# Kernel optimization log

Hardware: AMD Instinct MI355X
Metric: run time of the kernel (lower is better)

## Reference

```python
import jax, jax.numpy as jnp
import numpy as np

N_RAYS = 32768
HID = 64
MARCH_ITERS = 64
EPS = 1e-4
NEAR = 0.0
FAR = 1.0
T_FAR = 1.0
TPUT_B = 64
JITTER = 1.0 / TPUT_B  # fixed stand-in for random.random() * (2 / batch_size)


def _init_linear(key, fan_in, fan_out):
    kw, kb = jax.random.split(key)
    lim = 1.0 / np.sqrt(fan_in)
    W = jax.random.uniform(kw, (fan_in, fan_out), jnp.float32, -lim, lim)
    b = jax.random.uniform(kb, (fan_out,), jnp.float32, -lim, lim)
    return W, b


def setup_inputs() -> dict:
    key = jax.random.key(0)
    ks = jax.random.split(key, 6)
    rays = jax.random.normal(ks[0], (N_RAYS, 6), jnp.float32)
    W0, b0 = _init_linear(ks[1], 3, HID)
    W1, b1 = _init_linear(ks[2], HID, HID)
    W2, b2 = _init_linear(ks[3], HID, 1)
    Wr0, br0 = _init_linear(ks[4], 6, HID)
    Wr1, br1 = _init_linear(ks[5], HID, 3)
    return dict(rays=rays, W0=W0, b0=b0, W1=W1, b1=b1, W2=W2, b2=b2,
                Wr0=Wr0, br0=br0, Wr1=Wr1, br1=br1)


def _sdf(p, W0, b0, W1, b1, W2, b2):
    # p: [N, 3] -> signed distance [N, 1]
    h = jax.nn.relu(p @ W0 + b0)
    h = jax.nn.relu(h @ W1 + b1)
    return h @ W2 + b2


def _refl(p, d, Wr0, br0, Wr1, br1):
    # p, d: [N, 3] -> RGB [N, 3]
    h = jax.nn.relu(jnp.concatenate([p, d], axis=-1) @ Wr0 + br0)
    return jax.nn.sigmoid(h @ Wr1 + br1)


def reference(rays, W0, b0, W1, b1, W2, b2, Wr0, br0, Wr1, br1):
    r_o, r_d = rays[..., :3], rays[..., 3:]
    sdf = lambda p: _sdf(p, W0, b0, W1, b1, W2, b2)

    # --- sphere march (64 fixed iterations; early-exit break is a no-op
    # once all rays hit, since hit rays stop updating) ---
    hits0 = jnp.zeros(r_o.shape[:-1] + (1,), jnp.bool_)
    dist0 = jnp.full(r_o.shape[:-1] + (1,), NEAR, jnp.float32)

    def march(carry, _):
        hits, cd = carry
        d = sdf(r_o + r_d * cd)  # [N, 1]
        hits = hits | ((d < EPS) & (cd >= NEAR) & (cd <= FAR))
        cd = jnp.where(~hits, cd + d, cd)
        return (hits, cd), None

    (hit, t), _ = jax.lax.scan(march, (hits0, dist0), None, length=MARCH_ITERS)
    pts = r_o + r_d * t

    rgb = _refl(pts, r_d, Wr0, br0, Wr1, br1)
    rgb = jnp.where(hit, rgb, 0.0)  # out[~hit] = 0

    # --- throughput (index search under no_grad in the original) ---
    max_t = T_FAR + JITTER
    step = max_t / TPUT_B
    sg = jax.lax.stop_gradient
    sdf_ng = lambda p: _sdf(p, sg(W0), sg(b0), sg(W1), sg(b1), sg(W2), sg(b2))
    r_o_ng, r_d_ng = sg(r_o), sg(r_d)

    curr_min0 = sdf_ng(r_o_ng)[..., 0]          # [N]
    idxs0 = jnp.zeros_like(curr_min0, jnp.int32)

    def tloop(carry, i):
        cm, idxs = carry
        t_i = step * (i + 1).astype(jnp.float32)
        sd = sdf_ng(r_o_ng + t_i * r_d_ng)[..., 0]
        idxs = jnp.where(sd < cm, i + 1, idxs)
        return (jnp.minimum(cm, sd), idxs), None

    (_, idxs), _ = jax.lax.scan(tloop, (curr_min0, idxs0),
                                jnp.arange(TPUT_B, dtype=jnp.int32))

    best_pos = r_o + idxs[..., None].astype(jnp.float32) * step * r_d  # [N, 3]
    tput = sdf(best_pos)  # [N, 1], differentiable (outside no_grad in torch)

    return jnp.concatenate([rgb, tput], axis=-1)  # [N, 4]
```

## Files before the change

kernel.cpp:

```cpp
#include <hip/hip_runtime.h>
#include <math.h>

#define NRAYS        32768
#define MARCH_ITERS  64
#define EPS_         1e-4f
#define STEP_        ((1.0f + 1.0f/64.0f) / 64.0f)

typedef __attribute__((ext_vector_type(8)))  short    short8;
typedef __attribute__((ext_vector_type(4)))  float    float4v;
typedef __attribute__((ext_vector_type(2)))  float    float2v;
typedef __attribute__((ext_vector_type(4)))  unsigned uint4v;

__device__ __forceinline__ short8 mk_frag(unsigned p0, unsigned p1,
                                          unsigned p2, unsigned p3) {
    uint4v v = {p0, p1, p2, p3};
    return __builtin_bit_cast(short8, v);
}

__device__ __forceinline__ unsigned packbf(unsigned a, unsigned b) {
    return __builtin_amdgcn_perm(b, a, 0x07060302u);
}

struct Split2 { unsigned h, r; };
__device__ __forceinline__ Split2 split2(float x) {
    unsigned xu = __float_as_uint(x);
    float xh = __uint_as_float(xu & 0xFFFF0000u);
    float rr = x - xh;
    return { xu, __float_as_uint(rr) };
}

__device__ __forceinline__ float2v fma2(float2v a, float2v b, float2v c) {
    return __builtin_elementwise_fma(a, b, c);
}

__device__ __forceinline__ float xor16_sum(float x) {
    float p = __int_as_float(
        __builtin_amdgcn_ds_swizzle(__float_as_int(x), 0x401F));
    return x + p;
}
__device__ __forceinline__ float xor32_sum(float x) {
    return x + __shfl_xor(x, 32, 64);
}

__global__ __launch_bounds__(64)
__attribute__((amdgpu_waves_per_eu(2, 2)))
void sdf_w13_k(
    const float* __restrict__ rays,
    const float* __restrict__ W0,  const float* __restrict__ b0,
    const float* __restrict__ W1,  const float* __restrict__ b1,
    const float* __restrict__ W2,  const float* __restrict__ b2,
    const float* __restrict__ Wr0, const float* __restrict__ br0,
    const float* __restrict__ Wr1, const float* __restrict__ br1,
    float* __restrict__ out)
{
    const int lane = threadIdx.x;
    const int quad = lane >> 4;
    const int m    = lane & 15;
    const int rayBase = blockIdx.x * 16;

    const float* rp = rays + (rayBase + m) * 6;
    const float ox = rp[0], oy = rp[1], oz = rp[2];
    const float dx = rp[3], dy = rp[4], dz = rp[5];

    float2v a2[4][2], s2[4][2];
    #pragma unroll
    for (int t = 0; t < 4; ++t)
        #pragma unroll
        for (int p = 0; p < 2; ++p) {
            float av[2], sv[2];
            #pragma unroll
            for (int e = 0; e < 2; ++e) {
                int j = 32 * (t >> 1) + 8 * quad + 4 * (t & 1) + (2 * p + e);
                float w0c = W0[j], w1c = W0[64 + j], w2c = W0[128 + j];
                av[e] = fmaf(ox, w0c, fmaf(oy, w1c, fmaf(oz, w2c, b0[j])));
                sv[e] = fmaf(dx, w0c, fmaf(dy, w1c, dz * w2c));
            }
            a2[t][p] = (float2v){av[0], av[1]};
            s2[t][p] = (float2v){sv[0], sv[1]};
        }

    float4v b1v[4];
    float2v w2a[4], w2b[4];
    #pragma unroll
    for (int t = 0; t < 4; ++t) {
        int base = 16 * t + 4 * quad;
        b1v[t] = (float4v){b1[base], b1[base + 1], b1[base + 2], b1[base + 3]};
        w2a[t] = (float2v){W2[base], W2[base + 1]};
        w2b[t] = (float2v){W2[base + 2], W2[base + 3]};
    }
    const float b2s = b2[0];

    short8 A2h[2][4], A2m[2][4];
    #pragma unroll
    for (int h = 0; h < 2; ++h)
        #pragma unroll
        for (int t = 0; t < 4; ++t) {
            unsigned pm[4], ph[4];
            #pragma unroll
            for (int jp = 0; jp < 4; ++jp) {
                int k0 = 32 * h + quad * 8 + 2 * jp;
                int j2 = 16 * t + m;
                Split2 a = split2(W1[k0 * 64 + j2]);
                Split2 b = split2(W1[(k0 + 1) * 64 + j2]);
                pm[jp] = packbf(a.r, b.r);
                ph[jp] = packbf(a.h, b.h);
            }
            A2m[h][t] = mk_frag(pm[0], pm[1], pm[2], pm[3]);
            A2h[h][t] = mk_frag(ph[0], ph[1], ph[2], ph[3]);
        }

    const float2v z2 = {0.f, 0.f};
    auto front = [&](float cv, short8* BH, short8* BM) {
        const float2v c2 = {cv, cv};
        unsigned PH[4][2], PM[4][2];
        #pragma unroll
        for (int t = 0; t < 4; ++t) {
            float2v v01 = fma2(c2, s2[t][0], a2[t][0]);
            float2v v23 = fma2(c2, s2[t][1], a2[t][1]);
            v01 = __builtin_elementwise_max(v01, z2);
            v23 = __builtin_elementwise_max(v23, z2);
            unsigned u0 = __float_as_uint(v01.x), u1 = __float_as_uint(v01.y);
            unsigned u2 = __float_as_uint(v23.x), u3 = __float_as_uint(v23.y);
            PH[t][0] = packbf(u0, u1); PH[t][1] = packbf(u2, u3);
            float2v h01 = {__uint_as_float(u0 & 0xFFFF0000u),
                           __uint_as_float(u1 & 0xFFFF0000u)};
            float2v h23 = {__uint_as_float(u2 & 0xFFFF0000u),
                           __uint_as_float(u3 & 0xFFFF0000u)};
            float2v r01 = v01 - h01;
            float2v r23 = v23 - h23;
            PM[t][0] = packbf(__float_as_uint(r01.x), __float_as_uint(r01.y));
            PM[t][1] = packbf(__float_as_uint(r23.x), __float_as_uint(r23.y));
        }
        #pragma unroll
        for (int h = 0; h < 2; ++h) {
            BH[h] = mk_frag(PH[2 * h][0], PH[2 * h][1],
                            PH[2 * h + 1][0], PH[2 * h + 1][1]);
            BM[h] = mk_frag(PM[2 * h][0], PM[2 * h][1],
                            PM[2 * h + 1][0], PM[2 * h + 1][1]);
        }
    };

    auto l3 = [&](const float4v* C2) -> float {
        float2v q01 = {0.f, 0.f}, q23 = {0.f, 0.f};
        #pragma unroll
        for (int t = 0; t < 4; ++t) {
            float2v rel01 = __builtin_elementwise_max(
                (float2v){C2[t][0], C2[t][1]}, z2);
            float2v rel23 = __builtin_elementwise_max(
                (float2v){C2[t][2], C2[t][3]}, z2);
            q01 = fma2(rel01, w2a[t], q01);
            q23 = fma2(rel23, w2b[t], q23);
        }
        float part = (q01.x + q01.y) + (q23.x + q23.y);
        part = xor16_sum(part);
        part = xor32_sum(part);
        return b2s + part;
    };

    auto tputC2 = [&](const short8* BHt, const short8* BMt, float4v* C2t) {
        #pragma unroll
        for (int t = 0; t < 4; ++t)
            C2t[t] = __builtin_amdgcn_mfma_f32_16x16x32_bf16(
                A2h[0][t], BMt[0], b1v[t], 0, 0, 0);
        #pragma unroll
        for (int t = 0; t < 4; ++t)
            C2t[t] = __builtin_amdgcn_mfma_f32_16x16x32_bf16(
                A2h[1][t], BMt[1], C2t[t], 0, 0, 0);
        #pragma unroll
        for (int h = 0; h < 2; ++h)
            #pragma unroll
            for (int t = 0; t < 4; ++t)
                C2t[t] = __builtin_amdgcn_mfma_f32_16x16x32_bf16(
                    A2h[h][t], BHt[h], C2t[t], 0, 0, 0);
    };

    bool  hit = false;
    float cd  = 0.f;
    float cm  = 3.4e38f;
    int   i   = 0;

    short8 BHt[2], BMt[2];
    front(0.f, BHt, BMt);

    #pragma unroll 1
    for (; i < MARCH_ITERS; ++i) {
        if (__all(hit)) break;
        float4v C2t[4];
        tputC2(BHt, BMt, C2t);
        short8 BHtN[2], BMtN[2];
        front(STEP_ * (float)(i + 1), BHtN, BMtN);
        short8 BHm[2], BMm[2];
        front(cd, BHm, BMm);
        float4v C2m[4];
        #pragma unroll
        for (int t = 0; t < 4; ++t)
            C2m[t] = __builtin_amdgcn_mfma_f32_16x16x32_bf16(
                A2m[0][t], BHm[0], b1v[t], 0, 0, 0);
        #pragma unroll
        for (int t = 0; t < 4; ++t)
            C2m[t] = __builtin_amdgcn_mfma_f32_16x16x32_bf16(
                A2m[1][t], BHm[1], C2m[t], 0, 0, 0);
        #pragma unroll
        for (int h = 0; h < 2; ++h)
            #pragma unroll
            for (int t = 0; t < 4; ++t)
                C2m[t] = __builtin_amdgcn_mfma_f32_16x16x32_bf16(
                    A2h[h][t], BMm[h], C2m[t], 0, 0, 0);
        #pragma unroll
        for (int h = 0; h < 2; ++h)
            #pragma unroll
            for (int t = 0; t < 4; ++t)
                C2m[t] = __builtin_amdgcn_mfma_f32_16x16x32_bf16(
                    A2h[h][t], BHm[h], C2m[t], 0, 0, 0);
        float dm = l3(C2m);
        bool c = (dm < EPS_) && (cd >= 0.f) && (cd <= 1.f);
        hit = hit || c;
        if (!hit) cd += dm;
        cm = fminf(cm, l3(C2t));
        BHt[0] = BHtN[0]; BHt[1] = BHtN[1];
        BMt[0] = BMtN[0]; BMt[1] = BMtN[1];
    }

    #pragma unroll 1
    for (; i <= 64; ++i) {
        float4v C2t[4];
        tputC2(BHt, BMt, C2t);
        cm = fminf(cm, l3(C2t));
        if (i < 64)
            front(STEP_ * (float)(i + 1), BHt, BMt);
    }

    const float px = fmaf(dx, cd, ox), py = fmaf(dy, cd, oy), pz = fmaf(dz, cd, oz);
    float r0 = 0.f, r1 = 0.f, r2 = 0.f;
    #pragma unroll 4
    for (int jj = 0; jj < 16; ++jj) {
        int j = quad * 16 + jj;
        float a = fmaf(px, Wr0[j],
                  fmaf(py, Wr0[64 + j],
                  fmaf(pz, Wr0[128 + j],
                  fmaf(dx, Wr0[192 + j],
                  fmaf(dy, Wr0[256 + j],
                  fmaf(dz, Wr0[320 + j], br0[j]))))));
        a = fmaxf(a, 0.f);
        r0 = fmaf(a, Wr1[j * 3 + 0], r0);
        r1 = fmaf(a, Wr1[j * 3 + 1], r1);
        r2 = fmaf(a, Wr1[j * 3 + 2], r2);
    }
    r0 = xor16_sum(r0); r0 = xor32_sum(r0);
    r1 = xor16_sum(r1); r1 = xor32_sum(r1);
    r2 = xor16_sum(r2); r2 = xor32_sum(r2);
    r0 = 1.f / (1.f + expf(-(r0 + br1[0])));
    r1 = 1.f / (1.f + expf(-(r1 + br1[1])));
    r2 = 1.f / (1.f + expf(-(r2 + br1[2])));
    if (!hit) { r0 = 0.f; r1 = 0.f; r2 = 0.f; }
    if (lane < 16) {
        float4v o4 = {r0, r1, r2, cm};
        *reinterpret_cast<float4v*>(out + (rayBase + lane) * 4) = o4;
    }
}

extern "C" void kernel_launch(void* const* d_in, const int* in_sizes, int n_in,
                              void* d_out, int out_size, void* d_ws, size_t ws_size,
                              hipStream_t stream) {
    const float* rays = (const float*)d_in[0];
    const float* W0   = (const float*)d_in[1];
    const float* b0   = (const float*)d_in[2];
    const float* W1   = (const float*)d_in[3];
    const float* b1   = (const float*)d_in[4];
    const float* W2   = (const float*)d_in[5];
    const float* b2   = (const float*)d_in[6];
    const float* Wr0  = (const float*)d_in[7];
    const float* br0  = (const float*)d_in[8];
    const float* Wr1  = (const float*)d_in[9];
    const float* br1  = (const float*)d_in[10];
    float* out = (float*)d_out;

    hipLaunchKernelGGL(sdf_w13_k, dim3(NRAYS / 16), dim3(64), 0, stream,
                       rays, W0, b0, W1, b1, W2, b2, Wr0, br0, Wr1, br1, out);
}
```

Measured before the change: 171.8 us.

## Drop software-pipelined tput fragments, relax waves-per-EU, use permlane swaps for reductions

The throughput-search layer-1 fragments are now computed inside each iteration instead of being precomputed one iteration ahead. This removes the carried BHtN/BMtN registers. The waves_per_eu bound is relaxed from (2,2) to (2,8) so the compiler can trade registers for more resident waves. The cross-lane xor16/xor32 reductions use permlane16/32_swap builtins when they are available, replacing ds_swizzle and shfl. The tradeoff is less overlap between the front computation and the MFMA chain within a wave, in exchange for possibly higher occupancy.

```diff
diff --git a/kernel.cpp b/kernel.cpp
--- a/kernel.cpp
+++ b/kernel.cpp
@@ -10,6 +10,7 @@
 typedef __attribute__((ext_vector_type(4)))  float    float4v;
 typedef __attribute__((ext_vector_type(2)))  float    float2v;
 typedef __attribute__((ext_vector_type(4)))  unsigned uint4v;
+typedef __attribute__((ext_vector_type(2)))  unsigned uint2v;
 
 __device__ __forceinline__ short8 mk_frag(unsigned p0, unsigned p1,
                                           unsigned p2, unsigned p3) {
@@ -34,17 +35,29 @@
 }
 
 __device__ __forceinline__ float xor16_sum(float x) {
+#if __has_builtin(__builtin_amdgcn_permlane16_swap)
+    unsigned u = __float_as_uint(x);
+    uint2v r = __builtin_amdgcn_permlane16_swap(u, u, false, false);
+    return __uint_as_float(r.x) + __uint_as_float(r.y);
+#else
     float p = __int_as_float(
         __builtin_amdgcn_ds_swizzle(__float_as_int(x), 0x401F));
     return x + p;
+#endif
 }
 __device__ __forceinline__ float xor32_sum(float x) {
+#if __has_builtin(__builtin_amdgcn_permlane32_swap)
+    unsigned u = __float_as_uint(x);
+    uint2v r = __builtin_amdgcn_permlane32_swap(u, u, false, false);
+    return __uint_as_float(r.x) + __uint_as_float(r.y);
+#else
     return x + __shfl_xor(x, 32, 64);
+#endif
 }
 
 __global__ __launch_bounds__(64)
-__attribute__((amdgpu_waves_per_eu(2, 2)))
-void sdf_w13_k(
+__attribute__((amdgpu_waves_per_eu(2, 8)))
+void sdf_w15_k(
     const float* __restrict__ rays,
     const float* __restrict__ W0,  const float* __restrict__ b0,
     const float* __restrict__ W1,  const float* __restrict__ b1,
@@ -179,19 +192,15 @@
     float cm  = 3.4e38f;
     int   i   = 0;
 
-    short8 BHt[2], BMt[2];
-    front(0.f, BHt, BMt);
-
     #pragma unroll 1
-    for (; i < MARCH_ITERS; ++i) {
-        if (__all(hit)) break;
-        float4v C2t[4];
-        tputC2(BHt, BMt, C2t);
-        short8 BHtN[2], BMtN[2];
-        front(STEP_ * (float)(i + 1), BHtN, BMtN);
+    for (; i <= 64; ++i) {
+        if (i >= MARCH_ITERS || __all(hit)) break;
+        float ti = STEP_ * (float)i;
+        short8 BHt[2], BMt[2];
+        front(ti, BHt, BMt);
         short8 BHm[2], BMm[2];
         front(cd, BHm, BMm);
-        float4v C2m[4];
+        float4v C2m[4], C2t[4];
         #pragma unroll
         for (int t = 0; t < 4; ++t)
             C2m[t] = __builtin_amdgcn_mfma_f32_16x16x32_bf16(
@@ -212,22 +221,22 @@
             for (int t = 0; t < 4; ++t)
                 C2m[t] = __builtin_amdgcn_mfma_f32_16x16x32_bf16(
                     A2h[h][t], BHm[h], C2m[t], 0, 0, 0);
+        tputC2(BHt, BMt, C2t);
         float dm = l3(C2m);
         bool c = (dm < EPS_) && (cd >= 0.f) && (cd <= 1.f);
         hit = hit || c;
         if (!hit) cd += dm;
         cm = fminf(cm, l3(C2t));
-        BHt[0] = BHtN[0]; BHt[1] = BHtN[1];
-        BMt[0] = BMtN[0]; BMt[1] = BMtN[1];
     }
 
     #pragma unroll 1
     for (; i <= 64; ++i) {
+        float ti = STEP_ * (float)i;
+        short8 BHt[2], BMt[2];
+        front(ti, BHt, BMt);
         float4v C2t[4];
         tputC2(BHt, BMt, C2t);
         cm = fminf(cm, l3(C2t));
-        if (i < 64)
-            front(STEP_ * (float)(i + 1), BHt, BMt);
     }
 
     const float px = fmaf(dx, cd, ox), py = fmaf(dy, cd, oy), pz = fmaf(dz, cd, oz);
@@ -275,6 +284,6 @@
     const float* br1  = (const float*)d_in[10];
     float* out = (float*)d_out;
 
-    hipLaunchKernelGGL(sdf_w13_k, dim3(NRAYS / 16), dim3(64), 0, stream,
+    hipLaunchKernelGGL(sdf_w15_k, dim3(NRAYS / 16), dim3(64), 0, stream,
                        rays, W0, b0, W1, b1, W2, b2, Wr0, br0, Wr1, br1, out);
 }
```

New measurement: 165.8 us. 1.04x faster.
